# Optimization experiments

Measured on AMD Instinct MI355X. Metric: run time of the kernel, lower is better.

## Reference

```python
import jax, jax.numpy as jnp
import numpy as np

V_MIN = -10.0
V_MAX = 10.0
NUM_ATOMS = 251
B = 131072
N_OBS = 128
N_ACT = 32
HID = 512


def _ln(x, g, b, eps=1e-5):
    m = jnp.mean(x, axis=-1, keepdims=True)
    v = jnp.var(x, axis=-1, keepdims=True)
    return (x - m) * jax.lax.rsqrt(v + eps) * g + b


def setup_inputs() -> dict:
    key = jax.random.key(0)
    ks = jax.random.split(key, 16)

    def lin(k, fi, fo):
        kw, kb = jax.random.split(k)
        lim = 1.0 / np.sqrt(fi)
        W = jax.random.uniform(kw, (fi, fo), jnp.float32, -lim, lim)
        b = jax.random.uniform(kb, (fo,), jnp.float32, -lim, lim)
        return W, b

    W1, b1 = lin(ks[0], N_OBS + N_ACT, HID)
    W2, b2 = lin(ks[1], HID, HID // 2)
    W3, b3 = lin(ks[2], HID // 2, HID // 4)
    W4, b4 = lin(ks[3], HID // 4, NUM_ATOMS)

    return {
        "obs": jax.random.normal(ks[4], (B, N_OBS), jnp.float32),
        "actions": jax.random.normal(ks[5], (B, N_ACT), jnp.float32),
        "rewards": jax.random.normal(ks[6], (B,), jnp.float32),
        "bootstrap": (jax.random.uniform(ks[7], (B,)) > 0.05).astype(jnp.float32),
        "discount": jnp.full((B,), 0.99, jnp.float32),
        "q_support": jnp.linspace(V_MIN, V_MAX, NUM_ATOMS, dtype=jnp.float32),
        "W1": W1, "b1": b1, "g1": jnp.ones((HID,), jnp.float32), "be1": jnp.zeros((HID,), jnp.float32),
        "W2": W2, "b2": b2, "g2": jnp.ones((HID // 2,), jnp.float32), "be2": jnp.zeros((HID // 2,), jnp.float32),
        "W3": W3, "b3": b3, "g3": jnp.ones((HID // 4,), jnp.float32), "be3": jnp.zeros((HID // 4,), jnp.float32),
        "W4": W4, "b4": b4,
    }


def _net(obs, actions, W1, b1, g1, be1, W2, b2, g2, be2, W3, b3, g3, be3, W4, b4):
    x = jnp.concatenate([obs, actions], axis=1)
    x = jax.nn.silu(_ln(x @ W1 + b1, g1, be1))
    x = jax.nn.silu(_ln(x @ W2 + b2, g2, be2))
    x = jax.nn.silu(_ln(x @ W3 + b3, g3, be3))
    return x @ W4 + b4  # [B, NUM_ATOMS] logits


def reference(obs, actions, rewards, bootstrap, discount, q_support,
              W1, b1, g1, be1, W2, b2, g2, be2, W3, b3, g3, be3, W4, b4):
    # C51 categorical projection (DistributionalQNetwork.projection)
    delta_z = (V_MAX - V_MIN) / (NUM_ATOMS - 1)
    bsz = rewards.shape[0]
    target_z = rewards[:, None] + bootstrap[:, None] * discount[:, None] * q_support[None, :]
    target_z = jnp.clip(target_z, V_MIN, V_MAX)
    b = (target_z - V_MIN) / delta_z  # fractional bin positions [B, A]
    lower = jnp.floor(b).astype(jnp.int32)
    upper = jnp.ceil(b).astype(jnp.int32)
    is_integer = upper == lower
    lower_mask = (lower > 0) & is_integer
    upper_mask = (lower == 0) & is_integer
    lower = jnp.where(lower_mask, lower - 1, lower)
    upper = jnp.where(upper_mask, upper + 1, upper)

    logits = _net(obs, actions, W1, b1, g1, be1, W2, b2, g2, be2, W3, b3, g3, be3, W4, b4)
    next_dist = jax.nn.softmax(logits, axis=1)

    offset = (jnp.arange(bsz, dtype=jnp.int32) * NUM_ATOMS)[:, None]  # [B,1]
    max_index = bsz * NUM_ATOMS - 1
    li = jnp.clip((lower + offset).reshape(-1), 0, max_index)
    ui = jnp.clip((upper + offset).reshape(-1), 0, max_index)

    w_lo = (next_dist * (upper.astype(jnp.float32) - b)).reshape(-1)
    w_hi = (next_dist * (b - lower.astype(jnp.float32))).reshape(-1)

    proj = jnp.zeros((bsz * NUM_ATOMS,), next_dist.dtype)
    proj = proj.at[li].add(w_lo).at[ui].add(w_hi)
    return proj.reshape(bsz, NUM_ATOMS)
```

## Files before the change

### kernel.cpp

```cpp
#include <hip/hip_runtime.h>


#define THREADS 256
#define PREP_THREADS 256

typedef __attribute__((ext_vector_type(8))) short short8v;
typedef __attribute__((ext_vector_type(4))) float f32x4;

__device__ __forceinline__ unsigned short f2bf(float f) {
  union { float f; unsigned u; } v; v.f = f;
  unsigned u = v.u;
  u += 0x7fffu + ((u >> 16) & 1u);
  return (unsigned short)(u >> 16);
}
__device__ __forceinline__ unsigned pack2bf(float a, float b) {
  unsigned r;
  asm("v_cvt_pk_bf16_f32 %0, %1, %2" : "=v"(r) : "v"(a), "v"(b));
  return r;
}

__global__ void prep_kernel(const float* __restrict__ W1, const float* __restrict__ W2,
                            const float* __restrict__ W3, const float* __restrict__ W4,
                            unsigned short* __restrict__ ws) {
  int i = blockIdx.x * PREP_THREADS + threadIdx.x;
  if (i < 81920) {
    int n = i / 160, k = i - n * 160;
    ws[i] = f2bf(W1[k * 512 + n]);
  } else if (i < 212992) {
    int j = i - 81920; int n = j >> 9, k = j & 511;
    ws[i] = f2bf(W2[k * 256 + n]);
  } else if (i < 245760) {
    int j = i - 212992; int n = j >> 8, k = j & 255;
    ws[i] = f2bf(W3[k * 128 + n]);
  } else if (i < 278528) {
    int j = i - 245760; int n = j >> 7, k = j & 127;
    ws[i] = (n < 251) ? f2bf(W4[k * 251 + n]) : (unsigned short)0;
  }
}

#define OFF_R   0
#define OFF_ZS  32768
#define OFF_B4  33792
#define OFF_RED 34816
#define LDS_TOTAL 36096

template<int KD, int NFT, int FPG, int DEPTH>
__device__ __forceinline__ void gemm_w(const unsigned short* __restrict__ WT,
                                       const unsigned char* __restrict__ Hb,
                                       int fbase, f32x4 (&acc)[NFT][2]) {
  const int lane = threadIdx.x & 63;
  const int lm = lane & 15, kg = lane >> 4;
  constexpr int KS  = KD / 32;
  constexpr int G   = NFT / FPG;
  constexpr int NIT = KS * G;
  constexpr int PF  = DEPTH - 1;
  constexpr int PB  = DEPTH - 1;

  const int woff0 = (fbase + lm) * KD + kg * 8;
  int boff[2][2];
#pragma unroll
  for (int rt = 0; rt < 2; ++rt) {
    const int r = rt * 16 + lm;
    const int swz = (r & 7) << 4;
    const int base = r * (KD * 2) + kg * 16;
    boff[rt][0] = base ^ swz;
    boff[rt][1] = (base + 64) ^ swz;
  }

  short8v abuf[DEPTH][FPG];
  short8v bbuf[DEPTH][2];

#pragma unroll
  for (int ks = 0; ks < PB && ks < KS; ++ks) {
    const int koff = (ks >> 1) * 128;
#pragma unroll
    for (int rt = 0; rt < 2; ++rt)
      bbuf[ks % DEPTH][rt] = *(const short8v*)(Hb + boff[rt][ks & 1] + koff);
  }
#pragma unroll
  for (int p = 0; p < PF && p < NIT; ++p) {
    const int g = p % G, ks = p / G;
#pragma unroll
    for (int f = 0; f < FPG; ++f)
      abuf[p % DEPTH][f] =
          *(const short8v*)(WT + woff0 + (g * FPG + f) * (16 * KD) + ks * 32);
  }

#pragma unroll
  for (int it = 0; it < NIT; ++it) {
    const int ks = it / G, g = it % G;
    if (g == 0 && ks + PB < KS) {
      const int nks = ks + PB;
      const int koff = (nks >> 1) * 128;
#pragma unroll
      for (int rt = 0; rt < 2; ++rt)
        bbuf[nks % DEPTH][rt] = *(const short8v*)(Hb + boff[rt][nks & 1] + koff);
    }
    if (it + PF < NIT) {
      const int nit = it + PF;
      const int ng = nit % G, nks = nit / G;
#pragma unroll
      for (int f = 0; f < FPG; ++f)
        abuf[nit % DEPTH][f] =
            *(const short8v*)(WT + woff0 + (ng * FPG + f) * (16 * KD) + nks * 32);
    }
#pragma unroll
    for (int f = 0; f < FPG; ++f) {
      const int ft = g * FPG + f;
      acc[ft][0] = __builtin_amdgcn_mfma_f32_16x16x32_bf16(
          abuf[it % DEPTH][f], bbuf[ks % DEPTH][0], acc[ft][0], 0, 0, 0);
      acc[ft][1] = __builtin_amdgcn_mfma_f32_16x16x32_bf16(
          abuf[it % DEPTH][f], bbuf[ks % DEPTH][1], acc[ft][1], 0, 0, 0);
    }
  }
}

template<int ND, int NFT>
__device__ __forceinline__ void ln_silu_store(
    f32x4 (&acc)[NFT][2],
    const float* __restrict__ bias, const float* __restrict__ g,
    const float* __restrict__ be, unsigned char* __restrict__ Hb,
    float* __restrict__ redL, int fbase, int fq)
{
  const int lane = threadIdx.x & 63;
  const int lm = lane & 15, kg = lane >> 4;
  float s[2] = {0.f, 0.f}, q[2] = {0.f, 0.f};
#pragma unroll
  for (int ft = 0; ft < NFT; ++ft) {
    const int f0 = fbase + ft * 16 + kg * 4;
    const f32x4 bb = *(const f32x4*)(bias + f0);
#pragma unroll
    for (int rt = 0; rt < 2; ++rt)
#pragma unroll
      for (int rg = 0; rg < 4; ++rg) {
        float x = acc[ft][rt][rg] + bb[rg];
        acc[ft][rt][rg] = x;
        s[rt] += x; q[rt] += x * x;
      }
  }
#pragma unroll
  for (int rt = 0; rt < 2; ++rt) {
    s[rt] += __shfl_xor(s[rt], 16); s[rt] += __shfl_xor(s[rt], 32);
    q[rt] += __shfl_xor(q[rt], 16); q[rt] += __shfl_xor(q[rt], 32);
  }
  if (lane < 16) {
#pragma unroll
    for (int rt = 0; rt < 2; ++rt) {
      redL[(rt * 16 + lm) * 9 + fq * 2    ] = s[rt];
      redL[(rt * 16 + lm) * 9 + fq * 2 + 1] = q[rt];
    }
  }
  __syncthreads();
  float mean[2], rstd[2];
#pragma unroll
  for (int rt = 0; rt < 2; ++rt) {
    const int row = rt * 16 + lm;
    float S = 0.f, Q = 0.f;
#pragma unroll
    for (int w = 0; w < 4; ++w) {
      S += redL[row * 9 + w * 2];
      Q += redL[row * 9 + w * 2 + 1];
    }
    float m = S * (1.0f / ND);
    float v = Q * (1.0f / ND) - m * m;
    mean[rt] = m; rstd[rt] = rsqrtf(v + 1e-5f);
  }
#pragma unroll
  for (int ft = 0; ft < NFT; ++ft) {
    const int f0 = fbase + ft * 16 + kg * 4;
    const f32x4 g4 = *(const f32x4*)(g + f0);
    const f32x4 e4 = *(const f32x4*)(be + f0);
#pragma unroll
    for (int rt = 0; rt < 2; ++rt) {
      const int row = rt * 16 + lm;
      float h[4];
#pragma unroll
      for (int rg = 0; rg < 4; ++rg) {
        float y = (acc[ft][rt][rg] - mean[rt]) * rstd[rt] * g4[rg] + e4[rg];
        h[rg] = y * (1.0f / (1.0f + __expf(-y)));
      }
      uint2 w; w.x = pack2bf(h[0], h[1]); w.y = pack2bf(h[2], h[3]);
      int byte = row * (ND * 2) + f0 * 2;
      byte ^= ((row & 7) << 4);
      *(uint2*)(Hb + byte) = w;
    }
  }
}

__global__ __launch_bounds__(THREADS, 4) void fused_kernel(
    const float* __restrict__ obs, const float* __restrict__ actions,
    const float* __restrict__ rewards, const float* __restrict__ bootstrap,
    const float* __restrict__ discount, const float* __restrict__ q_support,
    const float* __restrict__ b1, const float* __restrict__ g1, const float* __restrict__ be1,
    const float* __restrict__ b2, const float* __restrict__ g2, const float* __restrict__ be2,
    const float* __restrict__ b3, const float* __restrict__ g3, const float* __restrict__ be3,
    const float* __restrict__ b4,
    const unsigned short* __restrict__ ws,
    float* __restrict__ out)
{
  __shared__ __align__(16) unsigned char smem[LDS_TOTAL];
  const int tid  = threadIdx.x;
  const int fq   = tid >> 6;
  const int lane = tid & 63;
  const int lm   = lane & 15;
  const int kg   = lane >> 4;
  const int row0 = blockIdx.x * 32;

  const unsigned short* W1T = ws;
  const unsigned short* W2T = ws + 81920;
  const unsigned short* W3T = ws + 212992;
  const unsigned short* W4T = ws + 245760;

  float* zsL  = (float*)(smem + OFF_ZS);
  float* b4L  = (float*)(smem + OFF_B4);
  float* redL = (float*)(smem + OFF_RED);

  float rw[2], bt[2], dc[2];
#pragma unroll
  for (int rt = 0; rt < 2; ++rt) {
    const int r = row0 + rt * 16 + lm;
    rw[rt] = rewards[r]; bt[rt] = bootstrap[r]; dc[rt] = discount[r];
  }

  zsL[tid] = (tid < 251) ? q_support[tid] : 0.f;
  b4L[tid] = (tid < 251) ? b4[tid] : 0.f;

  {
    unsigned char* Xb = smem + OFF_R;
#pragma unroll
    for (int it = 0; it < 5; ++it) {
      const int qq = it * THREADS + tid;
      const int r  = qq / 40;
      const int c4 = (qq - r * 40) * 4;
      float4 v;
      if (c4 < 128) v = *(const float4*)(obs + (size_t)(row0 + r) * 128 + c4);
      else          v = *(const float4*)(actions + (size_t)(row0 + r) * 32 + (c4 - 128));
      uint2 w; w.x = pack2bf(v.x, v.y); w.y = pack2bf(v.z, v.w);
      int byte = r * 320 + c4 * 2;
      byte ^= ((r & 7) << 4);
      *(uint2*)(Xb + byte) = w;
    }
  }
  __syncthreads();

  f32x4 acc1[8][2];
#pragma unroll
  for (int i = 0; i < 8; ++i) { acc1[i][0] = f32x4{0,0,0,0}; acc1[i][1] = f32x4{0,0,0,0}; }
  gemm_w<160, 8, 2, 2>(W1T, smem + OFF_R, fq * 128, acc1);
  ln_silu_store<512, 8>(acc1, b1, g1, be1, smem + OFF_R, redL, fq * 128, fq);
  __syncthreads();

  f32x4 acc2[4][2];
#pragma unroll
  for (int i = 0; i < 4; ++i) { acc2[i][0] = f32x4{0,0,0,0}; acc2[i][1] = f32x4{0,0,0,0}; }
  gemm_w<512, 4, 2, 3>(W2T, smem + OFF_R, fq * 64, acc2);
  ln_silu_store<256, 4>(acc2, b2, g2, be2, smem + OFF_R, redL, fq * 64, fq);
  __syncthreads();

  f32x4 acc3[2][2];
#pragma unroll
  for (int i = 0; i < 2; ++i) { acc3[i][0] = f32x4{0,0,0,0}; acc3[i][1] = f32x4{0,0,0,0}; }
  gemm_w<256, 2, 2, 3>(W3T, smem + OFF_R, fq * 32, acc3);
  ln_silu_store<128, 2>(acc3, b3, g3, be3, smem + OFF_R, redL, fq * 32, fq);
  __syncthreads();

  f32x4 acc4[4][2];
#pragma unroll
  for (int i = 0; i < 4; ++i) { acc4[i][0] = f32x4{0,0,0,0}; acc4[i][1] = f32x4{0,0,0,0}; }
  gemm_w<128, 4, 2, 3>(W4T, smem + OFF_R, fq * 64, acc4);

  float lv[4][2][4];
#pragma unroll
  for (int ft = 0; ft < 4; ++ft) {
    const int f0 = fq * 64 + ft * 16 + kg * 4;
    const f32x4 bb = *(const f32x4*)(b4L + f0);
#pragma unroll
    for (int rt = 0; rt < 2; ++rt)
#pragma unroll
      for (int rg = 0; rg < 4; ++rg) {
        const int f = f0 + rg;
        lv[ft][rt][rg] = (f < 251) ? (acc4[ft][rt][rg] + bb[rg]) : -1e30f;
      }
  }

#pragma unroll
  for (int rt = 0; rt < 2; ++rt) {
    float m = lv[0][rt][0];
#pragma unroll
    for (int ft = 0; ft < 4; ++ft)
#pragma unroll
      for (int rg = 0; rg < 4; ++rg) m = fmaxf(m, lv[ft][rt][rg]);
    m = fmaxf(m, __shfl_xor(m, 16));
    m = fmaxf(m, __shfl_xor(m, 32));
    if (lane < 16) redL[(rt * 16 + lm) * 5 + fq] = m;
  }
  __syncthreads();

  float* projL = (float*)(smem + OFF_R);
  for (int i = tid; i < 32 * 251; i += THREADS) projL[i] = 0.f;

  float gm[2];
#pragma unroll
  for (int rt = 0; rt < 2; ++rt) {
    const int row = rt * 16 + lm;
    float m = redL[row * 5];
#pragma unroll
    for (int w = 1; w < 4; ++w) m = fmaxf(m, redL[row * 5 + w]);
    gm[rt] = m;
  }
  __syncthreads();
#pragma unroll
  for (int rt = 0; rt < 2; ++rt) {
    float E = 0.f;
#pragma unroll
    for (int ft = 0; ft < 4; ++ft)
#pragma unroll
      for (int rg = 0; rg < 4; ++rg) {
        float e = __expf(lv[ft][rt][rg] - gm[rt]);
        lv[ft][rt][rg] = e;
        E += e;
      }
    E += __shfl_xor(E, 16); E += __shfl_xor(E, 32);
    if (lane < 16) redL[(rt * 16 + lm) * 5 + fq] = E;
  }
  __syncthreads();
  float inv[2];
#pragma unroll
  for (int rt = 0; rt < 2; ++rt) {
    const int row = rt * 16 + lm;
    float E = 0.f;
#pragma unroll
    for (int w = 0; w < 4; ++w) E += redL[row * 5 + w];
    inv[rt] = 1.0f / E;
  }

  constexpr float DZF = 20.0f / 250.0f;
  constexpr float INVDZ = 1.0f / DZF;
#pragma unroll
  for (int ft = 0; ft < 4; ++ft) {
    const int f0 = fq * 64 + ft * 16 + kg * 4;
    const f32x4 z4 = *(const f32x4*)(zsL + f0);
#pragma unroll
    for (int rt = 0; rt < 2; ++rt) {
      const int base = (rt * 16 + lm) * 251;
      const float bd = __fmul_rn(bt[rt], dc[rt]);
#pragma unroll
      for (int rg = 0; rg < 4; ++rg) {
        const int f = f0 + rg;
        if (f < 251) {
          const float p = lv[ft][rt][rg] * inv[rt];
          float t = __fadd_rn(rw[rt], __fmul_rn(bd, z4[rg]));
          t = fminf(fmaxf(t, -10.0f), 10.0f);
          const float bfr = __fmul_rn(__fsub_rn(t, -10.0f), INVDZ);
          const float fl = floorf(bfr), fu = ceilf(bfr);
          int l = (int)fl, u = (int)fu;
          if (fl == fu) { if (l > 0) --l; else ++u; }
          atomicAdd(projL + base + l, p * ((float)u - bfr));
          atomicAdd(projL + base + u, p * (bfr - (float)l));
        }
      }
    }
  }
  __syncthreads();

  const float4* ps = (const float4*)projL;
  float4* po = (float4*)(out + (size_t)row0 * 251);
  for (int i = tid; i < 2008; i += THREADS) po[i] = ps[i];
}

extern "C" void kernel_launch(void* const* d_in, const int* in_sizes, int n_in,
                              void* d_out, int out_size, void* d_ws, size_t ws_size,
                              hipStream_t stream) {
  const float* obs  = (const float*)d_in[0];
  const float* act  = (const float*)d_in[1];
  const float* rew  = (const float*)d_in[2];
  const float* boot = (const float*)d_in[3];
  const float* disc = (const float*)d_in[4];
  const float* zs   = (const float*)d_in[5];
  const float* W1   = (const float*)d_in[6];
  const float* b1   = (const float*)d_in[7];
  const float* g1   = (const float*)d_in[8];
  const float* be1  = (const float*)d_in[9];
  const float* W2   = (const float*)d_in[10];
  const float* b2   = (const float*)d_in[11];
  const float* g2   = (const float*)d_in[12];
  const float* be2  = (const float*)d_in[13];
  const float* W3   = (const float*)d_in[14];
  const float* b3   = (const float*)d_in[15];
  const float* g3   = (const float*)d_in[16];
  const float* be3  = (const float*)d_in[17];
  const float* W4   = (const float*)d_in[18];
  const float* b4   = (const float*)d_in[19];
  unsigned short* wsp = (unsigned short*)d_ws;

  const int Bn = in_sizes[2];
  prep_kernel<<<(278528 + PREP_THREADS - 1) / PREP_THREADS, PREP_THREADS, 0, stream>>>(
      W1, W2, W3, W4, wsp);
  fused_kernel<<<Bn / 32, THREADS, 0, stream>>>(obs, act, rew, boot, disc, zs,
      b1, g1, be1, b2, g2, be2, b3, g3, be3, b4, wsp, (float*)d_out);
}
```

Baseline: 489.6 us.

## Double rows per block to 64 with 8 waves splitting output features

Result: slower. 533.1 us (+8.9%).

```diff
diff --git a/kernel.cpp b/kernel.cpp
--- a/kernel.cpp
+++ b/kernel.cpp
@@ -1,7 +1,7 @@
 #include <hip/hip_runtime.h>
 
 
-#define THREADS 256
+#define THREADS 512
 #define PREP_THREADS 256
 
 typedef __attribute__((ext_vector_type(8))) short short8v;
@@ -39,27 +39,26 @@
 }
 
 #define OFF_R   0
-#define OFF_ZS  32768
-#define OFF_B4  33792
-#define OFF_RED 34816
-#define LDS_TOTAL 36096
+#define OFF_ZS  65536
+#define OFF_B4  66560
+#define OFF_RED 67584
+#define LDS_TOTAL 71936
 
 template<int KD, int NFT, int FPG, int DEPTH>
 __device__ __forceinline__ void gemm_w(const unsigned short* __restrict__ WT,
                                        const unsigned char* __restrict__ Hb,
-                                       int fbase, f32x4 (&acc)[NFT][2]) {
+                                       int fbase, f32x4 (&acc)[NFT][4]) {
   const int lane = threadIdx.x & 63;
   const int lm = lane & 15, kg = lane >> 4;
   constexpr int KS  = KD / 32;
   constexpr int G   = NFT / FPG;
   constexpr int NIT = KS * G;
   constexpr int PF  = DEPTH - 1;
-  constexpr int PB  = DEPTH - 1;
 
   const int woff0 = (fbase + lm) * KD + kg * 8;
-  int boff[2][2];
-#pragma unroll
-  for (int rt = 0; rt < 2; ++rt) {
+  int boff[4][2];
+#pragma unroll
+  for (int rt = 0; rt < 4; ++rt) {
     const int r = rt * 16 + lm;
     const int swz = (r & 7) << 4;
     const int base = r * (KD * 2) + kg * 16;
@@ -68,15 +67,8 @@
   }
 
   short8v abuf[DEPTH][FPG];
-  short8v bbuf[DEPTH][2];
-
-#pragma unroll
-  for (int ks = 0; ks < PB && ks < KS; ++ks) {
-    const int koff = (ks >> 1) * 128;
-#pragma unroll
-    for (int rt = 0; rt < 2; ++rt)
-      bbuf[ks % DEPTH][rt] = *(const short8v*)(Hb + boff[rt][ks & 1] + koff);
-  }
+  short8v bbuf[4];
+
 #pragma unroll
   for (int p = 0; p < PF && p < NIT; ++p) {
     const int g = p % G, ks = p / G;
@@ -89,12 +81,11 @@
 #pragma unroll
   for (int it = 0; it < NIT; ++it) {
     const int ks = it / G, g = it % G;
-    if (g == 0 && ks + PB < KS) {
-      const int nks = ks + PB;
-      const int koff = (nks >> 1) * 128;
-#pragma unroll
-      for (int rt = 0; rt < 2; ++rt)
-        bbuf[nks % DEPTH][rt] = *(const short8v*)(Hb + boff[rt][nks & 1] + koff);
+    if (g == 0) {
+      const int koff = (ks >> 1) * 128;
+#pragma unroll
+      for (int rt = 0; rt < 4; ++rt)
+        bbuf[rt] = *(const short8v*)(Hb + boff[rt][ks & 1] + koff);
     }
     if (it + PF < NIT) {
       const int nit = it + PF;
@@ -107,30 +98,30 @@
 #pragma unroll
     for (int f = 0; f < FPG; ++f) {
       const int ft = g * FPG + f;
-      acc[ft][0] = __builtin_amdgcn_mfma_f32_16x16x32_bf16(
-          abuf[it % DEPTH][f], bbuf[ks % DEPTH][0], acc[ft][0], 0, 0, 0);
-      acc[ft][1] = __builtin_amdgcn_mfma_f32_16x16x32_bf16(
-          abuf[it % DEPTH][f], bbuf[ks % DEPTH][1], acc[ft][1], 0, 0, 0);
+#pragma unroll
+      for (int rt = 0; rt < 4; ++rt)
+        acc[ft][rt] = __builtin_amdgcn_mfma_f32_16x16x32_bf16(
+            abuf[it % DEPTH][f], bbuf[rt], acc[ft][rt], 0, 0, 0);
     }
   }
 }
 
 template<int ND, int NFT>
 __device__ __forceinline__ void ln_silu_store(
-    f32x4 (&acc)[NFT][2],
+    f32x4 (&acc)[NFT][4],
     const float* __restrict__ bias, const float* __restrict__ g,
     const float* __restrict__ be, unsigned char* __restrict__ Hb,
     float* __restrict__ redL, int fbase, int fq)
 {
   const int lane = threadIdx.x & 63;
   const int lm = lane & 15, kg = lane >> 4;
-  float s[2] = {0.f, 0.f}, q[2] = {0.f, 0.f};
+  float s[4] = {0.f, 0.f, 0.f, 0.f}, q[4] = {0.f, 0.f, 0.f, 0.f};
 #pragma unroll
   for (int ft = 0; ft < NFT; ++ft) {
     const int f0 = fbase + ft * 16 + kg * 4;
     const f32x4 bb = *(const f32x4*)(bias + f0);
 #pragma unroll
-    for (int rt = 0; rt < 2; ++rt)
+    for (int rt = 0; rt < 4; ++rt)
 #pragma unroll
       for (int rg = 0; rg < 4; ++rg) {
         float x = acc[ft][rt][rg] + bb[rg];
@@ -139,27 +130,27 @@
       }
   }
 #pragma unroll
-  for (int rt = 0; rt < 2; ++rt) {
+  for (int rt = 0; rt < 4; ++rt) {
     s[rt] += __shfl_xor(s[rt], 16); s[rt] += __shfl_xor(s[rt], 32);
     q[rt] += __shfl_xor(q[rt], 16); q[rt] += __shfl_xor(q[rt], 32);
   }
   if (lane < 16) {
 #pragma unroll
-    for (int rt = 0; rt < 2; ++rt) {
-      redL[(rt * 16 + lm) * 9 + fq * 2    ] = s[rt];
-      redL[(rt * 16 + lm) * 9 + fq * 2 + 1] = q[rt];
-    }
-  }
-  __syncthreads();
-  float mean[2], rstd[2];
-#pragma unroll
-  for (int rt = 0; rt < 2; ++rt) {
+    for (int rt = 0; rt < 4; ++rt) {
+      redL[(rt * 16 + lm) * 17 + fq * 2    ] = s[rt];
+      redL[(rt * 16 + lm) * 17 + fq * 2 + 1] = q[rt];
+    }
+  }
+  __syncthreads();
+  float mean[4], rstd[4];
+#pragma unroll
+  for (int rt = 0; rt < 4; ++rt) {
     const int row = rt * 16 + lm;
     float S = 0.f, Q = 0.f;
 #pragma unroll
-    for (int w = 0; w < 4; ++w) {
-      S += redL[row * 9 + w * 2];
-      Q += redL[row * 9 + w * 2 + 1];
+    for (int w = 0; w < 8; ++w) {
+      S += redL[row * 17 + w * 2];
+      Q += redL[row * 17 + w * 2 + 1];
     }
     float m = S * (1.0f / ND);
     float v = Q * (1.0f / ND) - m * m;
@@ -171,7 +162,7 @@
     const f32x4 g4 = *(const f32x4*)(g + f0);
     const f32x4 e4 = *(const f32x4*)(be + f0);
 #pragma unroll
-    for (int rt = 0; rt < 2; ++rt) {
+    for (int rt = 0; rt < 4; ++rt) {
       const int row = rt * 16 + lm;
       float h[4];
 #pragma unroll
@@ -204,7 +195,7 @@
   const int lane = tid & 63;
   const int lm   = lane & 15;
   const int kg   = lane >> 4;
-  const int row0 = blockIdx.x * 32;
+  const int row0 = blockIdx.x * 64;
 
   const unsigned short* W1T = ws;
   const unsigned short* W2T = ws + 81920;
@@ -215,15 +206,10 @@
   float* b4L  = (float*)(smem + OFF_B4);
   float* redL = (float*)(smem + OFF_RED);
 
-  float rw[2], bt[2], dc[2];
-#pragma unroll
-  for (int rt = 0; rt < 2; ++rt) {
-    const int r = row0 + rt * 16 + lm;
-    rw[rt] = rewards[r]; bt[rt] = bootstrap[r]; dc[rt] = discount[r];
-  }
-
-  zsL[tid] = (tid < 251) ? q_support[tid] : 0.f;
-  b4L[tid] = (tid < 251) ? b4[tid] : 0.f;
+  if (tid < 256) {
+    zsL[tid] = (tid < 251) ? q_support[tid] : 0.f;
+    b4L[tid] = (tid < 251) ? b4[tid] : 0.f;
+  }
 
   {
     unsigned char* Xb = smem + OFF_R;
@@ -243,39 +229,52 @@
   }
   __syncthreads();
 
-  f32x4 acc1[8][2];
-#pragma unroll
-  for (int i = 0; i < 8; ++i) { acc1[i][0] = f32x4{0,0,0,0}; acc1[i][1] = f32x4{0,0,0,0}; }
-  gemm_w<160, 8, 2, 2>(W1T, smem + OFF_R, fq * 128, acc1);
-  ln_silu_store<512, 8>(acc1, b1, g1, be1, smem + OFF_R, redL, fq * 128, fq);
-  __syncthreads();
-
-  f32x4 acc2[4][2];
-#pragma unroll
-  for (int i = 0; i < 4; ++i) { acc2[i][0] = f32x4{0,0,0,0}; acc2[i][1] = f32x4{0,0,0,0}; }
-  gemm_w<512, 4, 2, 3>(W2T, smem + OFF_R, fq * 64, acc2);
-  ln_silu_store<256, 4>(acc2, b2, g2, be2, smem + OFF_R, redL, fq * 64, fq);
-  __syncthreads();
-
-  f32x4 acc3[2][2];
-#pragma unroll
-  for (int i = 0; i < 2; ++i) { acc3[i][0] = f32x4{0,0,0,0}; acc3[i][1] = f32x4{0,0,0,0}; }
-  gemm_w<256, 2, 2, 3>(W3T, smem + OFF_R, fq * 32, acc3);
-  ln_silu_store<128, 2>(acc3, b3, g3, be3, smem + OFF_R, redL, fq * 32, fq);
-  __syncthreads();
-
-  f32x4 acc4[4][2];
-#pragma unroll
-  for (int i = 0; i < 4; ++i) { acc4[i][0] = f32x4{0,0,0,0}; acc4[i][1] = f32x4{0,0,0,0}; }
-  gemm_w<128, 4, 2, 3>(W4T, smem + OFF_R, fq * 64, acc4);
-
-  float lv[4][2][4];
-#pragma unroll
-  for (int ft = 0; ft < 4; ++ft) {
-    const int f0 = fq * 64 + ft * 16 + kg * 4;
+  f32x4 acc1[4][4];
+#pragma unroll
+  for (int i = 0; i < 4; ++i)
+#pragma unroll
+    for (int j = 0; j < 4; ++j) acc1[i][j] = f32x4{0.f, 0.f, 0.f, 0.f};
+  gemm_w<160, 4, 2, 3>(W1T, smem + OFF_R, fq * 64, acc1);
+  ln_silu_store<512, 4>(acc1, b1, g1, be1, smem + OFF_R, redL, fq * 64, fq);
+  __syncthreads();
+
+  f32x4 acc2[2][4];
+#pragma unroll
+  for (int i = 0; i < 2; ++i)
+#pragma unroll
+    for (int j = 0; j < 4; ++j) acc2[i][j] = f32x4{0.f, 0.f, 0.f, 0.f};
+  gemm_w<512, 2, 2, 3>(W2T, smem + OFF_R, fq * 32, acc2);
+  ln_silu_store<256, 2>(acc2, b2, g2, be2, smem + OFF_R, redL, fq * 32, fq);
+  __syncthreads();
+
+  f32x4 acc3[1][4];
+#pragma unroll
+  for (int j = 0; j < 4; ++j) acc3[0][j] = f32x4{0.f, 0.f, 0.f, 0.f};
+  gemm_w<256, 1, 1, 3>(W3T, smem + OFF_R, fq * 16, acc3);
+  ln_silu_store<128, 1>(acc3, b3, g3, be3, smem + OFF_R, redL, fq * 16, fq);
+  __syncthreads();
+
+  f32x4 acc4[2][4];
+#pragma unroll
+  for (int i = 0; i < 2; ++i)
+#pragma unroll
+    for (int j = 0; j < 4; ++j) acc4[i][j] = f32x4{0.f, 0.f, 0.f, 0.f};
+  gemm_w<128, 2, 2, 3>(W4T, smem + OFF_R, fq * 32, acc4);
+
+  float rw[4], bt[4], dc[4];
+#pragma unroll
+  for (int rt = 0; rt < 4; ++rt) {
+    const int r = row0 + rt * 16 + lm;
+    rw[rt] = rewards[r]; bt[rt] = bootstrap[r]; dc[rt] = discount[r];
+  }
+
+  float lv[2][4][4];
+#pragma unroll
+  for (int ft = 0; ft < 2; ++ft) {
+    const int f0 = fq * 32 + ft * 16 + kg * 4;
     const f32x4 bb = *(const f32x4*)(b4L + f0);
 #pragma unroll
-    for (int rt = 0; rt < 2; ++rt)
+    for (int rt = 0; rt < 4; ++rt)
 #pragma unroll
       for (int rg = 0; rg < 4; ++rg) {
         const int f = f0 + rg;
@@ -284,36 +283,36 @@
   }
 
 #pragma unroll
-  for (int rt = 0; rt < 2; ++rt) {
+  for (int rt = 0; rt < 4; ++rt) {
     float m = lv[0][rt][0];
 #pragma unroll
-    for (int ft = 0; ft < 4; ++ft)
+    for (int ft = 0; ft < 2; ++ft)
 #pragma unroll
       for (int rg = 0; rg < 4; ++rg) m = fmaxf(m, lv[ft][rt][rg]);
     m = fmaxf(m, __shfl_xor(m, 16));
     m = fmaxf(m, __shfl_xor(m, 32));
-    if (lane < 16) redL[(rt * 16 + lm) * 5 + fq] = m;
+    if (lane < 16) redL[(rt * 16 + lm) * 9 + fq] = m;
   }
   __syncthreads();
 
   float* projL = (float*)(smem + OFF_R);
-  for (int i = tid; i < 32 * 251; i += THREADS) projL[i] = 0.f;
-
-  float gm[2];
-#pragma unroll
-  for (int rt = 0; rt < 2; ++rt) {
+  for (int i = tid; i < 64 * 251; i += THREADS) projL[i] = 0.f;
+
+  float gm[4];
+#pragma unroll
+  for (int rt = 0; rt < 4; ++rt) {
     const int row = rt * 16 + lm;
-    float m = redL[row * 5];
-#pragma unroll
-    for (int w = 1; w < 4; ++w) m = fmaxf(m, redL[row * 5 + w]);
+    float m = redL[row * 9];
+#pragma unroll
+    for (int w = 1; w < 8; ++w) m = fmaxf(m, redL[row * 9 + w]);
     gm[rt] = m;
   }
   __syncthreads();
 #pragma unroll
-  for (int rt = 0; rt < 2; ++rt) {
+  for (int rt = 0; rt < 4; ++rt) {
     float E = 0.f;
 #pragma unroll
-    for (int ft = 0; ft < 4; ++ft)
+    for (int ft = 0; ft < 2; ++ft)
 #pragma unroll
       for (int rg = 0; rg < 4; ++rg) {
         float e = __expf(lv[ft][rt][rg] - gm[rt]);
@@ -321,27 +320,27 @@
         E += e;
       }
     E += __shfl_xor(E, 16); E += __shfl_xor(E, 32);
-    if (lane < 16) redL[(rt * 16 + lm) * 5 + fq] = E;
-  }
-  __syncthreads();
-  float inv[2];
-#pragma unroll
-  for (int rt = 0; rt < 2; ++rt) {
+    if (lane < 16) redL[(rt * 16 + lm) * 9 + fq] = E;
+  }
+  __syncthreads();
+  float inv[4];
+#pragma unroll
+  for (int rt = 0; rt < 4; ++rt) {
     const int row = rt * 16 + lm;
     float E = 0.f;
 #pragma unroll
-    for (int w = 0; w < 4; ++w) E += redL[row * 5 + w];
+    for (int w = 0; w < 8; ++w) E += redL[row * 9 + w];
     inv[rt] = 1.0f / E;
   }
 
   constexpr float DZF = 20.0f / 250.0f;
   constexpr float INVDZ = 1.0f / DZF;
 #pragma unroll
-  for (int ft = 0; ft < 4; ++ft) {
-    const int f0 = fq * 64 + ft * 16 + kg * 4;
+  for (int ft = 0; ft < 2; ++ft) {
+    const int f0 = fq * 32 + ft * 16 + kg * 4;
     const f32x4 z4 = *(const f32x4*)(zsL + f0);
 #pragma unroll
-    for (int rt = 0; rt < 2; ++rt) {
+    for (int rt = 0; rt < 4; ++rt) {
       const int base = (rt * 16 + lm) * 251;
       const float bd = __fmul_rn(bt[rt], dc[rt]);
 #pragma unroll
@@ -365,7 +364,7 @@
 
   const float4* ps = (const float4*)projL;
   float4* po = (float4*)(out + (size_t)row0 * 251);
-  for (int i = tid; i < 2008; i += THREADS) po[i] = ps[i];
+  for (int i = tid; i < 4016; i += THREADS) po[i] = ps[i];
 }
 
 extern "C" void kernel_launch(void* const* d_in, const int* in_sizes, int n_in,
@@ -396,6 +395,6 @@
   const int Bn = in_sizes[2];
   prep_kernel<<<(278528 + PREP_THREADS - 1) / PREP_THREADS, PREP_THREADS, 0, stream>>>(
       W1, W2, W3, W4, wsp);
-  fused_kernel<<<Bn / 32, THREADS, 0, stream>>>(obs, act, rew, boot, disc, zs,
+  fused_kernel<<<Bn / 64, THREADS, 0, stream>>>(obs, act, rew, boot, disc, zs,
       b1, g1, be1, b2, g2, be2, b3, g3, be3, b4, wsp, (float*)d_out);
 }
```

## Stage layer 2-4 weights into LDS via async global_load_lds double buffering

Applied to the files above, without the earlier changes.

Result: slower. 524.2 us (+7.1%).

```diff
diff --git a/kernel.cpp b/kernel.cpp
--- a/kernel.cpp
+++ b/kernel.cpp
@@ -17,6 +17,18 @@
   unsigned r;
   asm("v_cvt_pk_bf16_f32 %0, %1, %2" : "=v"(r) : "v"(a), "v"(b));
   return r;
+}
+
+__device__ __forceinline__ void gload16(const void* g, void* l) {
+  __builtin_amdgcn_global_load_lds(
+      (const __attribute__((address_space(1))) unsigned int*)g,
+      (__attribute__((address_space(3))) unsigned int*)l, 16, 0, 0);
+}
+template<int N>
+__device__ __forceinline__ void wait_vmcnt() {
+  if constexpr (N == 0)      asm volatile("s_waitcnt vmcnt(0)" ::: "memory");
+  else if constexpr (N == 2) asm volatile("s_waitcnt vmcnt(2)" ::: "memory");
+  else if constexpr (N == 4) asm volatile("s_waitcnt vmcnt(4)" ::: "memory");
 }
 
 __global__ void prep_kernel(const float* __restrict__ W1, const float* __restrict__ W2,
@@ -27,22 +39,32 @@
     int n = i / 160, k = i - n * 160;
     ws[i] = f2bf(W1[k * 512 + n]);
   } else if (i < 212992) {
-    int j = i - 81920; int n = j >> 9, k = j & 511;
+    int j = i - 81920;
+    int e = j & 7, lane = (j >> 3) & 63, ftg = (j >> 9) & 15, ks = j >> 13;
+    int n = ftg * 16 + (lane & 15);
+    int k = ks * 32 + ((lane >> 4) << 3) + e;
     ws[i] = f2bf(W2[k * 256 + n]);
   } else if (i < 245760) {
-    int j = i - 212992; int n = j >> 8, k = j & 255;
+    int j = i - 212992;
+    int e = j & 7, lane = (j >> 3) & 63, ftg = (j >> 9) & 7, ks = j >> 12;
+    int n = ftg * 16 + (lane & 15);
+    int k = ks * 32 + ((lane >> 4) << 3) + e;
     ws[i] = f2bf(W3[k * 128 + n]);
   } else if (i < 278528) {
-    int j = i - 245760; int n = j >> 7, k = j & 127;
+    int j = i - 245760;
+    int e = j & 7, lane = (j >> 3) & 63, ftg = (j >> 9) & 15, ks = j >> 13;
+    int n = ftg * 16 + (lane & 15);
+    int k = ks * 32 + ((lane >> 4) << 3) + e;
     ws[i] = (n < 251) ? f2bf(W4[k * 251 + n]) : (unsigned short)0;
   }
 }
 
 #define OFF_R   0
-#define OFF_ZS  32768
-#define OFF_B4  33792
-#define OFF_RED 34816
-#define LDS_TOTAL 36096
+#define OFF_W   32768
+#define OFF_ZS  65536
+#define OFF_B4  66560
+#define OFF_RED 67584
+#define LDS_TOTAL 68736
 
 template<int KD, int NFT, int FPG, int DEPTH>
 __device__ __forceinline__ void gemm_w(const unsigned short* __restrict__ WT,
@@ -54,7 +76,6 @@
   constexpr int G   = NFT / FPG;
   constexpr int NIT = KS * G;
   constexpr int PF  = DEPTH - 1;
-  constexpr int PB  = DEPTH - 1;
 
   const int woff0 = (fbase + lm) * KD + kg * 8;
   int boff[2][2];
@@ -66,12 +87,10 @@
     boff[rt][0] = base ^ swz;
     boff[rt][1] = (base + 64) ^ swz;
   }
-
   short8v abuf[DEPTH][FPG];
   short8v bbuf[DEPTH][2];
-
-#pragma unroll
-  for (int ks = 0; ks < PB && ks < KS; ++ks) {
+#pragma unroll
+  for (int ks = 0; ks < PF && ks < KS; ++ks) {
     const int koff = (ks >> 1) * 128;
 #pragma unroll
     for (int rt = 0; rt < 2; ++rt)
@@ -85,12 +104,11 @@
       abuf[p % DEPTH][f] =
           *(const short8v*)(WT + woff0 + (g * FPG + f) * (16 * KD) + ks * 32);
   }
-
 #pragma unroll
   for (int it = 0; it < NIT; ++it) {
     const int ks = it / G, g = it % G;
-    if (g == 0 && ks + PB < KS) {
-      const int nks = ks + PB;
+    if (g == 0 && ks + PF < KS) {
+      const int nks = ks + PF;
       const int koff = (nks >> 1) * 128;
 #pragma unroll
       for (int rt = 0; rt < 2; ++rt)
@@ -111,6 +129,59 @@
           abuf[it % DEPTH][f], bbuf[ks % DEPTH][0], acc[ft][0], 0, 0, 0);
       acc[ft][1] = __builtin_amdgcn_mfma_f32_16x16x32_bf16(
           abuf[it % DEPTH][f], bbuf[ks % DEPTH][1], acc[ft][1], 0, 0, 0);
+    }
+  }
+}
+
+template<int KD, int NFT>
+__device__ __forceinline__ void gemm_staged(const unsigned short* __restrict__ WS,
+                                            const unsigned char* __restrict__ Hact,
+                                            unsigned char* __restrict__ wbuf,
+                                            int fq, f32x4 (&acc)[NFT][2]) {
+  constexpr int KS = KD / 32;
+  constexpr int CSTRIDE = 4 * NFT * 512;
+  const int lane = threadIdx.x & 63;
+  const int lm = lane & 15, kg = lane >> 4;
+  int boff[2][2];
+#pragma unroll
+  for (int rt = 0; rt < 2; ++rt) {
+    const int r = rt * 16 + lm;
+    const int swz = (r & 7) << 4;
+    const int base = r * (KD * 2) + kg * 16;
+    boff[rt][0] = base ^ swz;
+    boff[rt][1] = (base + 64) ^ swz;
+  }
+  const unsigned short* gbase = WS + (size_t)fq * (NFT * 512) + (size_t)lane * 8;
+
+#pragma unroll
+  for (int c = 0; c < 2 && c < KS; ++c)
+#pragma unroll
+    for (int j = 0; j < NFT; ++j)
+      gload16(gbase + (size_t)c * CSTRIDE + j * 512,
+              wbuf + (c & 1) * (NFT * 1024) + j * 1024);
+
+#pragma unroll
+  for (int c = 0; c < KS; ++c) {
+    if (c + 1 < KS) wait_vmcnt<NFT>(); else wait_vmcnt<0>();
+    short8v a[NFT], b[2];
+#pragma unroll
+    for (int ft = 0; ft < NFT; ++ft)
+      a[ft] = *(const short8v*)(wbuf + (c & 1) * (NFT * 1024) + ft * 1024 + lane * 16);
+    const int koff = (c >> 1) * 128;
+#pragma unroll
+    for (int rt = 0; rt < 2; ++rt)
+      b[rt] = *(const short8v*)(Hact + boff[rt][c & 1] + koff);
+#pragma unroll
+    for (int ft = 0; ft < NFT; ++ft) {
+      acc[ft][0] = __builtin_amdgcn_mfma_f32_16x16x32_bf16(a[ft], b[0], acc[ft][0], 0, 0, 0);
+      acc[ft][1] = __builtin_amdgcn_mfma_f32_16x16x32_bf16(a[ft], b[1], acc[ft][1], 0, 0, 0);
+    }
+    __builtin_amdgcn_sched_barrier(0);
+    if (c + 2 < KS) {
+#pragma unroll
+      for (int j = 0; j < NFT; ++j)
+        gload16(gbase + (size_t)(c + 2) * CSTRIDE + j * 512,
+                wbuf + (c & 1) * (NFT * 1024) + j * 1024);
     }
   }
 }
@@ -187,7 +258,7 @@
   }
 }
 
-__global__ __launch_bounds__(THREADS, 4) void fused_kernel(
+__global__ __launch_bounds__(THREADS, 2) void fused_kernel(
     const float* __restrict__ obs, const float* __restrict__ actions,
     const float* __restrict__ rewards, const float* __restrict__ bootstrap,
     const float* __restrict__ discount, const float* __restrict__ q_support,
@@ -207,13 +278,14 @@
   const int row0 = blockIdx.x * 32;
 
   const unsigned short* W1T = ws;
-  const unsigned short* W2T = ws + 81920;
-  const unsigned short* W3T = ws + 212992;
-  const unsigned short* W4T = ws + 245760;
+  const unsigned short* W2S = ws + 81920;
+  const unsigned short* W3S = ws + 212992;
+  const unsigned short* W4S = ws + 245760;
 
   float* zsL  = (float*)(smem + OFF_ZS);
   float* b4L  = (float*)(smem + OFF_B4);
   float* redL = (float*)(smem + OFF_RED);
+  unsigned char* wbuf = smem + OFF_W + fq * 8192;
 
   float rw[2], bt[2], dc[2];
 #pragma unroll
@@ -221,7 +293,6 @@
     const int r = row0 + rt * 16 + lm;
     rw[rt] = rewards[r]; bt[rt] = bootstrap[r]; dc[rt] = discount[r];
   }
-
   zsL[tid] = (tid < 251) ? q_support[tid] : 0.f;
   b4L[tid] = (tid < 251) ? b4[tid] : 0.f;
 
@@ -246,28 +317,28 @@
   f32x4 acc1[8][2];
 #pragma unroll
   for (int i = 0; i < 8; ++i) { acc1[i][0] = f32x4{0,0,0,0}; acc1[i][1] = f32x4{0,0,0,0}; }
-  gemm_w<160, 8, 2, 2>(W1T, smem + OFF_R, fq * 128, acc1);
+  gemm_w<160, 8, 2, 3>(W1T, smem + OFF_R, fq * 128, acc1);
   ln_silu_store<512, 8>(acc1, b1, g1, be1, smem + OFF_R, redL, fq * 128, fq);
   __syncthreads();
 
   f32x4 acc2[4][2];
 #pragma unroll
   for (int i = 0; i < 4; ++i) { acc2[i][0] = f32x4{0,0,0,0}; acc2[i][1] = f32x4{0,0,0,0}; }
-  gemm_w<512, 4, 2, 3>(W2T, smem + OFF_R, fq * 64, acc2);
+  gemm_staged<512, 4>(W2S, smem + OFF_R, wbuf, fq, acc2);
   ln_silu_store<256, 4>(acc2, b2, g2, be2, smem + OFF_R, redL, fq * 64, fq);
   __syncthreads();
 
   f32x4 acc3[2][2];
 #pragma unroll
   for (int i = 0; i < 2; ++i) { acc3[i][0] = f32x4{0,0,0,0}; acc3[i][1] = f32x4{0,0,0,0}; }
-  gemm_w<256, 2, 2, 3>(W3T, smem + OFF_R, fq * 32, acc3);
+  gemm_staged<256, 2>(W3S, smem + OFF_R, wbuf, fq, acc3);
   ln_silu_store<128, 2>(acc3, b3, g3, be3, smem + OFF_R, redL, fq * 32, fq);
   __syncthreads();
 
   f32x4 acc4[4][2];
 #pragma unroll
   for (int i = 0; i < 4; ++i) { acc4[i][0] = f32x4{0,0,0,0}; acc4[i][1] = f32x4{0,0,0,0}; }
-  gemm_w<128, 4, 2, 3>(W4T, smem + OFF_R, fq * 64, acc4);
+  gemm_staged<128, 4>(W4S, smem + OFF_R, wbuf, fq, acc4);
 
   float lv[4][2][4];
 #pragma unroll
```
